# Optimization experiments

Hardware: AMD Instinct MI355X
Metric: run time of the kernel (lower is better)

The kernel has to match this reference:

```python
import jax, jax.numpy as jnp
import numpy as np

TAU = 0.6  # BGK relaxation time (>= 0.5 per __post_init__ stability check)
# D2Q9 lattice: velocities, weights, opposite-direction indices
E = np.array([[0, 0], [1, 0], [0, 1], [-1, 0], [0, -1],
              [1, 1], [-1, 1], [-1, -1], [1, -1]], dtype=np.int32)
W = np.array([4.0 / 9] + [1.0 / 9] * 4 + [1.0 / 36] * 4, dtype=np.float32)
OPP = np.array([0, 3, 4, 1, 2, 7, 8, 5, 6], dtype=np.int32)


def setup_inputs() -> dict:
    key = jax.random.key(0)
    k1, k2, k3 = jax.random.split(key, 3)
    nx, ny = 2048, 2048
    f = jax.random.uniform(k1, (nx, ny, 9), dtype=jnp.float32)  # positive populations
    rho = jnp.sum(f, axis=-1)                                    # consistent density
    u = 0.05 * jax.random.normal(k2, (nx, ny, 2), dtype=jnp.float32)  # low-Ma velocity
    obstacle_mask = jax.random.uniform(k3, (nx, ny)) < 0.01      # sparse solid cells
    return {"f": f, "rho": rho, "u": u, "obstacle_mask": obstacle_mask}


def _equilibrium(rho, u):
    # feq_i = w_i * rho * (1 + 3 e.u + 4.5 (e.u)^2 - 1.5 u.u)
    e = jnp.asarray(E, jnp.float32)
    w = jnp.asarray(W)
    eu = jnp.einsum('xyd,qd->xyq', u, e)              # [nx, ny, 9]
    usq = jnp.sum(u * u, axis=-1, keepdims=True)       # [nx, ny, 1]
    return w * rho[..., None] * (1.0 + 3.0 * eu + 4.5 * eu * eu - 1.5 * usq)


def reference(f, rho, u, obstacle_mask):
    # --- collide (BGK) ---
    feq = _equilibrium(rho, u)
    f_star = f - (f - feq) / TAU
    # --- stream: roll each direction by its lattice velocity (lattice not shifted) ---
    f_new = jnp.stack(
        [jnp.roll(f_star[..., i], shift=(int(E[i, 0]), int(E[i, 1])), axis=(0, 1))
         for i in range(9)],
        axis=-1,
    )
    # --- obstacle bounce-back: solid cells reflect post-collision populations ---
    f_bb = f_star[..., jnp.asarray(OPP)]
    f_new = jnp.where(obstacle_mask[..., None], f_bb, f_new)
    # --- lift macro fields from post-stream distributions ---
    rho_new = jnp.sum(f_new, axis=-1)
    e = jnp.asarray(E, jnp.float32)
    u_new = jnp.einsum('xyq,qd->xyd', f_new, e) / rho_new[..., None]
    # pack (f_new [..9], rho_new [..1], u_new [..2]) -> [nx, ny, 12]
    return jnp.concatenate([f_new, rho_new[..., None], u_new], axis=-1)
```

## Files before the change

kernel.cpp:

```cpp
#include <hip/hip_runtime.h>


#define NX 2048
#define NY 2048
#define WRAP 2047
#define TR 8
#define TC 64
#define NT 512
#define HCELLS 660
#define RS 608
#define LDSWORDS 6656

typedef float floatx4 __attribute__((ext_vector_type(4)));

__global__ __launch_bounds__(NT, 8) void lbm_step_kernel(
    const float* __restrict__ f,
    const float* __restrict__ rho,
    const float* __restrict__ u,
    const int*   __restrict__ mask,
    float*       __restrict__ out)
{
    __shared__ __align__(16) float buf[LDSWORDS];

    const int tid = threadIdx.x;
    const int y0 = blockIdx.x * TC;
    const int x0 = blockIdx.y * TR;

    const float2* __restrict__ u2 = reinterpret_cast<const float2*>(u);

    floatx4 bulkv[3];
    int bulkdst[3] = {-1, -1, -1};
    #pragma unroll
    for (int it = 0; it < 3; ++it) {
        const int k4 = tid + it * NT;
        if (k4 < 1440) {
            const int row  = (unsigned)k4 / 144u;
            const int col4 = k4 - row * 144;
            const int xr   = (x0 - 1 + row) & WRAP;
            const int srcf = (xr * NY + y0) * 9 + col4 * 4;
            bulkv[it]   = *reinterpret_cast<const floatx4*>(f + srcf);
            bulkdst[it] = row * RS + col4 * 4;
        }
    }
    float edgev = 0.0f; int edgedst = -1;
    if (tid < 180) {
        const int side = tid >= 90;
        const int er   = side ? tid - 90 : tid;
        const int rowE = (unsigned)er / 9u;
        const int i    = er - rowE * 9;
        const int xr   = (x0 - 1 + rowE) & WRAP;
        const int yc   = side ? ((y0 + TC) & WRAP) : ((y0 - 1) & WRAP);
        edgev   = f[(xr * NY + yc) * 9 + i];
        edgedst = rowE * RS + (side ? 585 : 576) + i;
    }
    float rr[2]; float2 uu[2]; int cbase[2] = {-1, -1};
    #pragma unroll
    for (int it = 0; it < 2; ++it) {
        const int k = tid + it * NT;
        if (k < HCELLS) {
            const int hr = (unsigned)k / 66u;
            const int hc = k - hr * 66;
            const int xr = (x0 - 1 + hr) & WRAP;
            const int yc = (y0 - 1 + hc) & WRAP;
            const int g  = xr * NY + yc;
            rr[it] = rho[g];
            uu[it] = u2[g];
            cbase[it] = hr * RS + (hc == 0 ? 576 : (hc == 65 ? 585 : (hc - 1) * 9));
        }
    }
    const int r = tid >> 6;
    const int c = tid & 63;
    const int m = mask[(x0 + r) * NY + (y0 + c)];

    #pragma unroll
    for (int it = 0; it < 3; ++it)
        if (bulkdst[it] >= 0)
            *reinterpret_cast<floatx4*>(&buf[bulkdst[it]]) = bulkv[it];
    if (edgedst >= 0) buf[edgedst] = edgev;
    __syncthreads();

    const float ITAU = 1.0f / 0.6f;
    const float OMT  = 1.0f - ITAU;
    #pragma unroll
    for (int it = 0; it < 2; ++it) {
        if (cbase[it] >= 0) {
            const int b0 = cbase[it];
            float fi[9];
            #pragma unroll
            for (int i = 0; i < 9; ++i) fi[i] = buf[b0 + i];
            const float rn = rr[it];
            const float ux = uu[it].x, uy = uu[it].y;
            const float C  = 1.0f - 1.5f * (ux * ux + uy * uy);
            const float a  = 3.0f * ux, b = 3.0f * uy;
            const float p  = a + b, q = a - b;
            const float ha = 0.5f * a * a, hb = 0.5f * b * b;
            const float hp = 0.5f * p * p, hq = 0.5f * q * q;
            const float Pm = rn * (4.0f / 9.0f);
            const float Ps = rn * (1.0f / 9.0f);
            const float Pd = rn * (1.0f / 36.0f);
            float feq[9];
            feq[0] = Pm * C;
            feq[1] = Ps * (C + a + ha);
            feq[2] = Ps * (C + b + hb);
            feq[3] = Ps * (C - a + ha);
            feq[4] = Ps * (C - b + hb);
            feq[5] = Pd * (C + p + hp);
            feq[6] = Pd * (C - q + hq);
            feq[7] = Pd * (C - p + hp);
            feq[8] = Pd * (C + q + hq);
            #pragma unroll
            for (int i = 0; i < 9; ++i)
                buf[b0 + i] = fmaf(feq[i], ITAU, OMT * fi[i]);
        }
    }
    __syncthreads();

    const int colmid = c * 9;
    const int colL   = (c == 0)  ? 576 : (c - 1) * 9;
    const int colR   = (c == 63) ? 585 : (c + 1) * 9;
    const int rA = r * RS;
    const int rB = rA + RS;
    const int rC = rB + RS;

    float fn[9];
    fn[0] = buf[rB + colmid + 0];
    fn[1] = buf[rA + colmid + 1];
    fn[2] = buf[rB + colL   + 2];
    fn[3] = buf[rC + colmid + 3];
    fn[4] = buf[rB + colR   + 4];
    fn[5] = buf[rA + colL   + 5];
    fn[6] = buf[rC + colL   + 6];
    fn[7] = buf[rC + colR   + 7];
    fn[8] = buf[rA + colR   + 8];
    if (m) {
        const int ob = rB + colmid;
        const int opp9[9] = {0, 3, 4, 1, 2, 7, 8, 5, 6};
        #pragma unroll
        for (int i = 0; i < 9; ++i) fn[i] = buf[ob + opp9[i]];
    }

    const float rhon = fn[0] + fn[1] + fn[2] + fn[3] + fn[4]
                     + fn[5] + fn[6] + fn[7] + fn[8];
    const float irho = __builtin_amdgcn_rcpf(rhon);
    const float uxn = (fn[1] - fn[3] + fn[5] - fn[6] - fn[7] + fn[8]) * irho;
    const float uyn = (fn[2] - fn[4] + fn[5] + fn[6] - fn[7] - fn[8]) * irho;

    __syncthreads();

    {
        const int b0 = tid * 13;
        #pragma unroll
        for (int i = 0; i < 9; ++i) buf[b0 + i] = fn[i];
        buf[b0 + 9]  = rhon;
        buf[b0 + 10] = uxn;
        buf[b0 + 11] = uyn;
    }
    __syncthreads();

    #pragma unroll
    for (int it = 0; it < 3; ++it) {
        const int k4 = tid + it * NT;
        const unsigned r2  = (unsigned)k4 / 192u;
        const int      rem = k4 - (int)r2 * 192;
        const unsigned cc  = (unsigned)rem / 3u;
        const int      q   = rem - (int)cc * 3;
        const int lbase = (int)r2 * (TC * 13) + (int)cc * 13 + q * 4;
        floatx4 v;
        v.x = buf[lbase + 0];
        v.y = buf[lbase + 1];
        v.z = buf[lbase + 2];
        v.w = buf[lbase + 3];
        const size_t obase = ((size_t)(x0 + (int)r2) * NY + y0) * 12 + (size_t)rem * 4;
        __builtin_nontemporal_store(v, reinterpret_cast<floatx4*>(out + obase));
    }
}

extern "C" void kernel_launch(void* const* d_in, const int* in_sizes, int n_in,
                              void* d_out, int out_size, void* d_ws, size_t ws_size,
                              hipStream_t stream) {
    const float* f    = (const float*)d_in[0];
    const float* rho  = (const float*)d_in[1];
    const float* u    = (const float*)d_in[2];
    const int*   mask = (const int*)d_in[3];
    float* out = (float*)d_out;

    dim3 block(NT, 1, 1);
    dim3 grid(NY / TC, NX / TR, 1);
    lbm_step_kernel<<<grid, block, 0, stream>>>(f, rho, u, mask, out);
}
```

Baseline: 349.0 us.

## Process four row tiles per block with register double-buffered prefetch

Each block now loops over four 8-row tiles instead of one. The next tile's populations, macro fields and mask are prefetched into registers while the current tile is collided and streamed. The output is staged in a separate LDS buffer and written per warp, which removes one barrier per tile and moves address math out of the loop. The halo rows are still reloaded for every tile, and the extra LDS and registers lower occupancy (launch bound 6), so there is less parallelism for hiding latency.

```diff
diff --git a/kernel.cpp b/kernel.cpp
--- a/kernel.cpp
+++ b/kernel.cpp
@@ -7,89 +7,127 @@
 #define TR 8
 #define TC 64
 #define NT 512
-#define HCELLS 660
+#define TILES 4
 #define RS 608
-#define LDSWORDS 6656
+#define FSTARW 6080
+#define STAGEW 6656
 
 typedef float floatx4 __attribute__((ext_vector_type(4)));
 
-__global__ __launch_bounds__(NT, 8) void lbm_step_kernel(
+#define LOADT(tt, ss) do {                                                     \
+    const int xadd_ = (tt) * TR;                                               \
+    _Pragma("unroll")                                                          \
+    for (int it_ = 0; it_ < 3; ++it_) if (bvalid[it_]) {                       \
+        const int xr_ = (brow[it_] + xadd_) & WRAP;                            \
+        bv[ss][it_] = *reinterpret_cast<const floatx4*>(f + xr_ * 18432 + bgcol[it_]); } \
+    if (eval_) { const int xr_ = (erow + xadd_) & WRAP;                        \
+        ev[ss] = f[xr_ * 18432 + egcol]; }                                     \
+    _Pragma("unroll")                                                          \
+    for (int it_ = 0; it_ < 2; ++it_) if (cvalid[it_]) {                       \
+        const int xr_ = (crow[it_] + xadd_) & WRAP;                            \
+        const int g_ = xr_ * NY + cgcol[it_];                                  \
+        rr[ss][it_] = rho[g_]; uu[ss][it_] = u2[g_]; }                         \
+    { const int xr_ = (mrow + xadd_) & WRAP;                                   \
+      mk[ss] = mask[xr_ * NY + y0 + c]; }                                      \
+} while (0)
+
+__global__ __launch_bounds__(NT, 6) void lbm_step_kernel(
     const float* __restrict__ f,
     const float* __restrict__ rho,
     const float* __restrict__ u,
     const int*   __restrict__ mask,
     float*       __restrict__ out)
 {
-    __shared__ __align__(16) float buf[LDSWORDS];
+    __shared__ __align__(16) float fstar[FSTARW];
+    __shared__ __align__(16) float stg[STAGEW];
 
     const int tid = threadIdx.x;
     const int y0 = blockIdx.x * TC;
-    const int x0 = blockIdx.y * TR;
+    const int xbase = blockIdx.y * (TR * TILES);
 
     const float2* __restrict__ u2 = reinterpret_cast<const float2*>(u);
 
-    floatx4 bulkv[3];
-    int bulkdst[3] = {-1, -1, -1};
+    int brow[3], bldst[3], bgcol[3]; bool bvalid[3];
     #pragma unroll
     for (int it = 0; it < 3; ++it) {
         const int k4 = tid + it * NT;
-        if (k4 < 1440) {
-            const int row  = (unsigned)k4 / 144u;
-            const int col4 = k4 - row * 144;
-            const int xr   = (x0 - 1 + row) & WRAP;
-            const int srcf = (xr * NY + y0) * 9 + col4 * 4;
-            bulkv[it]   = *reinterpret_cast<const floatx4*>(f + srcf);
-            bulkdst[it] = row * RS + col4 * 4;
-        }
-    }
-    float edgev = 0.0f; int edgedst = -1;
-    if (tid < 180) {
+        bvalid[it] = (k4 < 1440);
+        const int row = (unsigned)k4 / 144u;
+        const int col4 = k4 - row * 144;
+        brow[it]  = xbase - 1 + row;
+        bldst[it] = row * RS + col4 * 4;
+        bgcol[it] = y0 * 9 + col4 * 4;
+    }
+    const bool eval_ = (tid < 180);
+    int erow = 0, edst = 0, egcol = 0;
+    if (eval_) {
         const int side = tid >= 90;
         const int er   = side ? tid - 90 : tid;
         const int rowE = (unsigned)er / 9u;
-        const int i    = er - rowE * 9;
-        const int xr   = (x0 - 1 + rowE) & WRAP;
-        const int yc   = side ? ((y0 + TC) & WRAP) : ((y0 - 1) & WRAP);
-        edgev   = f[(xr * NY + yc) * 9 + i];
-        edgedst = rowE * RS + (side ? 585 : 576) + i;
-    }
-    float rr[2]; float2 uu[2]; int cbase[2] = {-1, -1};
+        const int iE   = er - rowE * 9;
+        erow  = xbase - 1 + rowE;
+        edst  = rowE * RS + (side ? 585 : 576) + iE;
+        const int yc = side ? ((y0 + TC) & WRAP) : ((y0 - 1) & WRAP);
+        egcol = yc * 9 + iE;
+    }
+    int crow[2], cbase[2], cgcol[2]; bool cvalid[2];
     #pragma unroll
     for (int it = 0; it < 2; ++it) {
         const int k = tid + it * NT;
-        if (k < HCELLS) {
-            const int hr = (unsigned)k / 66u;
-            const int hc = k - hr * 66;
-            const int xr = (x0 - 1 + hr) & WRAP;
-            const int yc = (y0 - 1 + hc) & WRAP;
-            const int g  = xr * NY + yc;
-            rr[it] = rho[g];
-            uu[it] = u2[g];
-            cbase[it] = hr * RS + (hc == 0 ? 576 : (hc == 65 ? 585 : (hc - 1) * 9));
-        }
-    }
-    const int r = tid >> 6;
+        cvalid[it] = (k < 660);
+        const int hr = (unsigned)k / 66u;
+        const int hc = k - hr * 66;
+        crow[it]  = xbase - 1 + hr;
+        cbase[it] = hr * RS + (hc == 0 ? 576 : (hc == 65 ? 585 : (hc - 1) * 9));
+        cgcol[it] = (y0 - 1 + hc) & WRAP;
+    }
+    const int w = tid >> 6;
     const int c = tid & 63;
-    const int m = mask[(x0 + r) * NY + (y0 + c)];
-
-    #pragma unroll
-    for (int it = 0; it < 3; ++it)
-        if (bulkdst[it] >= 0)
-            *reinterpret_cast<floatx4*>(&buf[bulkdst[it]]) = bulkv[it];
-    if (edgedst >= 0) buf[edgedst] = edgev;
-    __syncthreads();
+    const int mrow = xbase + w;
+    const int colmid = c * 9;
+    const int colL = (c == 0)  ? 576 : (c - 1) * 9;
+    const int colR = (c == 63) ? 585 : (c + 1) * 9;
+    const int rA = w * RS, rB2 = rA + RS, rC2 = rB2 + RS;
+    const int sbase = tid * 13;
+    int lread[3], ocol[3];
+    #pragma unroll
+    for (int it = 0; it < 3; ++it) {
+        const int k4w = c + it * 64;
+        const int cc = (unsigned)k4w / 3u;
+        const int q  = k4w - cc * 3;
+        lread[it] = w * 832 + cc * 13 + q * 4;
+        ocol[it]  = y0 * 12 + k4w * 4;
+    }
 
     const float ITAU = 1.0f / 0.6f;
     const float OMT  = 1.0f - ITAU;
-    #pragma unroll
-    for (int it = 0; it < 2; ++it) {
-        if (cbase[it] >= 0) {
+
+    floatx4 bv[2][3]; float ev[2]; float rr[2][2]; float2 uu[2][2]; int mk[2];
+
+    LOADT(0, 0);
+
+    #pragma unroll
+    for (int t = 0; t < TILES; ++t) {
+        const int s = t & 1;
+
+        #pragma unroll
+        for (int it = 0; it < 3; ++it)
+            if (bvalid[it]) *reinterpret_cast<floatx4*>(&fstar[bldst[it]]) = bv[s][it];
+        if (eval_) fstar[edst] = ev[s];
+
+        if (t + 1 < TILES) {
+            if (s == 0) LOADT(t + 1, 1); else LOADT(t + 1, 0);
+        }
+        __syncthreads();
+
+        #pragma unroll
+        for (int it = 0; it < 2; ++it) if (cvalid[it]) {
             const int b0 = cbase[it];
             float fi[9];
             #pragma unroll
-            for (int i = 0; i < 9; ++i) fi[i] = buf[b0 + i];
-            const float rn = rr[it];
-            const float ux = uu[it].x, uy = uu[it].y;
+            for (int i = 0; i < 9; ++i) fi[i] = fstar[b0 + i];
+            const float rn = rr[s][it];
+            const float ux = uu[s][it].x, uy = uu[s][it].y;
             const float C  = 1.0f - 1.5f * (ux * ux + uy * uy);
             const float a  = 3.0f * ux, b = 3.0f * uy;
             const float p  = a + b, q = a - b;
@@ -110,68 +148,49 @@
             feq[8] = Pd * (C + q + hq);
             #pragma unroll
             for (int i = 0; i < 9; ++i)
-                buf[b0 + i] = fmaf(feq[i], ITAU, OMT * fi[i]);
-        }
-    }
-    __syncthreads();
-
-    const int colmid = c * 9;
-    const int colL   = (c == 0)  ? 576 : (c - 1) * 9;
-    const int colR   = (c == 63) ? 585 : (c + 1) * 9;
-    const int rA = r * RS;
-    const int rB = rA + RS;
-    const int rC = rB + RS;
-
-    float fn[9];
-    fn[0] = buf[rB + colmid + 0];
-    fn[1] = buf[rA + colmid + 1];
-    fn[2] = buf[rB + colL   + 2];
-    fn[3] = buf[rC + colmid + 3];
-    fn[4] = buf[rB + colR   + 4];
-    fn[5] = buf[rA + colL   + 5];
-    fn[6] = buf[rC + colL   + 6];
-    fn[7] = buf[rC + colR   + 7];
-    fn[8] = buf[rA + colR   + 8];
-    if (m) {
-        const int ob = rB + colmid;
-        const int opp9[9] = {0, 3, 4, 1, 2, 7, 8, 5, 6};
-        #pragma unroll
-        for (int i = 0; i < 9; ++i) fn[i] = buf[ob + opp9[i]];
-    }
-
-    const float rhon = fn[0] + fn[1] + fn[2] + fn[3] + fn[4]
-                     + fn[5] + fn[6] + fn[7] + fn[8];
-    const float irho = __builtin_amdgcn_rcpf(rhon);
-    const float uxn = (fn[1] - fn[3] + fn[5] - fn[6] - fn[7] + fn[8]) * irho;
-    const float uyn = (fn[2] - fn[4] + fn[5] + fn[6] - fn[7] - fn[8]) * irho;
-
-    __syncthreads();
-
-    {
-        const int b0 = tid * 13;
-        #pragma unroll
-        for (int i = 0; i < 9; ++i) buf[b0 + i] = fn[i];
-        buf[b0 + 9]  = rhon;
-        buf[b0 + 10] = uxn;
-        buf[b0 + 11] = uyn;
-    }
-    __syncthreads();
-
-    #pragma unroll
-    for (int it = 0; it < 3; ++it) {
-        const int k4 = tid + it * NT;
-        const unsigned r2  = (unsigned)k4 / 192u;
-        const int      rem = k4 - (int)r2 * 192;
-        const unsigned cc  = (unsigned)rem / 3u;
-        const int      q   = rem - (int)cc * 3;
-        const int lbase = (int)r2 * (TC * 13) + (int)cc * 13 + q * 4;
-        floatx4 v;
-        v.x = buf[lbase + 0];
-        v.y = buf[lbase + 1];
-        v.z = buf[lbase + 2];
-        v.w = buf[lbase + 3];
-        const size_t obase = ((size_t)(x0 + (int)r2) * NY + y0) * 12 + (size_t)rem * 4;
-        __builtin_nontemporal_store(v, reinterpret_cast<floatx4*>(out + obase));
+                fstar[b0 + i] = fmaf(feq[i], ITAU, OMT * fi[i]);
+        }
+        __syncthreads();
+
+        float fn[9];
+        fn[0] = fstar[rB2 + colmid + 0];
+        fn[1] = fstar[rA  + colmid + 1];
+        fn[2] = fstar[rB2 + colL   + 2];
+        fn[3] = fstar[rC2 + colmid + 3];
+        fn[4] = fstar[rB2 + colR   + 4];
+        fn[5] = fstar[rA  + colL   + 5];
+        fn[6] = fstar[rC2 + colL   + 6];
+        fn[7] = fstar[rC2 + colR   + 7];
+        fn[8] = fstar[rA  + colR   + 8];
+        if (mk[s]) {
+            const int ob = rB2 + colmid;
+            fn[0] = fstar[ob + 0]; fn[1] = fstar[ob + 3]; fn[2] = fstar[ob + 4];
+            fn[3] = fstar[ob + 1]; fn[4] = fstar[ob + 2]; fn[5] = fstar[ob + 7];
+            fn[6] = fstar[ob + 8]; fn[7] = fstar[ob + 5]; fn[8] = fstar[ob + 6];
+        }
+        __syncthreads();
+
+        const float rhon = fn[0] + fn[1] + fn[2] + fn[3] + fn[4]
+                         + fn[5] + fn[6] + fn[7] + fn[8];
+        const float irho = __builtin_amdgcn_rcpf(rhon);
+        const float uxn = (fn[1] - fn[3] + fn[5] - fn[6] - fn[7] + fn[8]) * irho;
+        const float uyn = (fn[2] - fn[4] + fn[5] + fn[6] - fn[7] - fn[8]) * irho;
+
+        #pragma unroll
+        for (int i = 0; i < 9; ++i) stg[sbase + i] = fn[i];
+        stg[sbase + 9]  = rhon;
+        stg[sbase + 10] = uxn;
+        stg[sbase + 11] = uyn;
+        const int xorow = (xbase + t * TR + w) * 24576;
+        #pragma unroll
+        for (int it = 0; it < 3; ++it) {
+            floatx4 v;
+            v.x = stg[lread[it] + 0];
+            v.y = stg[lread[it] + 1];
+            v.z = stg[lread[it] + 2];
+            v.w = stg[lread[it] + 3];
+            __builtin_nontemporal_store(v, reinterpret_cast<floatx4*>(out + xorow + ocol[it]));
+        }
     }
 }
 
@@ -185,6 +204,6 @@
     float* out = (float*)d_out;
 
     dim3 block(NT, 1, 1);
-    dim3 grid(NY / TC, NX / TR, 1);
+    dim3 grid(NY / TC, NX / (TR * TILES), 1);
     lbm_step_kernel<<<grid, block, 0, stream>>>(f, rho, u, mask, out);
 }
```

Result: slower. 400.2 us (+14.7%).
